# Optimization experiments

Measured on AMD Instinct MI355X. Metric: run time of the kernel, lower is better.

## Reference

```python
import jax, jax.numpy as jnp
import numpy as np

NEG = -1e30  # mask value safe for logsumexp/max
HALF_POS = 4   # positive window: [t-4, t+4)
HALF_ALL = 16  # combined window: [t-16, t+16) (pos + 12 negatives each side)


def _normalize(x, axis=-1, eps=1e-12):
    # matches torch F.normalize: x / max(||x||, eps)
    n = jnp.linalg.norm(x, axis=axis, keepdims=True)
    return x / jnp.maximum(n, eps)


def _banded_logits(q, k, temperature):
    # q, k: [B, T, D] (normalized). Returns logits [B, T, W], valid mask, pos mask.
    B, T, D = q.shape
    offsets = jnp.arange(-HALF_ALL, HALF_ALL)          # [W=32]
    j = jnp.arange(T)[:, None] + offsets[None, :]      # [T, W] absolute indices
    valid = (j >= 0) & (j < T)                         # combined (pos+neg) window
    jc = jnp.clip(j, 0, T - 1)
    kg = k[:, jc, :]                                   # [B, T, W, D]
    logits = jnp.einsum('btd,btwd->btw', q, kg) / temperature
    pos = valid & (offsets >= -HALF_POS)[None, :] & (offsets < HALF_POS)[None, :]
    return logits, valid, pos


def _direction(q, k, temperature):
    logits, valid, pos = _banded_logits(q, k, temperature)
    lse_all = jax.nn.logsumexp(jnp.where(valid, logits, NEG), axis=2)  # [B, T]
    lse_pos = jax.nn.logsumexp(jnp.where(pos, logits, NEG), axis=2)    # [B, T]
    # per-t loss is mean over batch; summed over t
    loss_sum = jnp.sum(jnp.mean(lse_all - lse_pos, axis=0))
    max_all = jnp.max(jnp.where(valid, logits, NEG), axis=2)
    max_pos = jnp.max(jnp.where(pos, logits, NEG), axis=2)
    # argmax falls in positive block (positives listed first -> ties go positive)
    correct = jnp.sum((max_pos >= max_all).astype(jnp.float32))
    return loss_sum, correct


def setup_inputs() -> dict:
    key = jax.random.key(0)
    k1, k2 = jax.random.split(key)
    B, T, D = 16, 4096, 128
    return {
        'motion_feature': jax.random.normal(k1, (B, T, D), dtype=jnp.float32),
        'audio_feature': jax.random.normal(k2, (B, T, D), dtype=jnp.float32),
    }


def reference(motion_feature, audio_feature):
    temperature = 0.1
    B, T, D = motion_feature.shape
    m = _normalize(motion_feature, axis=2)
    a = _normalize(audio_feature, axis=2)
    m2a_loss, m2a_correct = _direction(m, a, temperature)
    a2m_loss, a2m_correct = _direction(a, m, temperature)
    final_loss = (m2a_loss + a2m_loss) / (2 * T)
    total_correct = (m2a_correct + a2m_correct) / (2 * T * B)
    return final_loss, total_correct
```

## Files before the change

### kernel.cpp

```cpp
#include <hip/hip_runtime.h>
#include <hip/hip_bf16.h>

typedef __attribute__((ext_vector_type(8))) short bf16x8;
typedef __attribute__((ext_vector_type(4))) float f32x4;

#define T_DIM 4096
#define B_DIM 16
#define D_DIM 128
#define TILE 64
#define NTILE 4
#define ROWS 96
#define SROW 136
#define NEGV -1e30f
#define NBLK 256
#define SCALE (1.0f / 131072.0f)

#define LDS_BARRIER() asm volatile("s_waitcnt lgkmcnt(0)\n\ts_barrier" ::: "memory")

__global__ __launch_bounds__(512, 2) void lcl_main(
    const float* __restrict__ mot, const float* __restrict__ aud,
    float* __restrict__ ws)
{
    __shared__ unsigned short sm[ROWS * SROW];
    __shared__ unsigned short sa[ROWS * SROW];
    __shared__ float invM[ROWS], invA[ROWS];
    __shared__ float redL[8], redC[8];

    const int tid  = threadIdx.x;
    const int lane = tid & 63;
    const int wv   = tid >> 6;
    const int g32  = tid >> 5;
    const int l32  = tid & 31;

    const int lin = blockIdx.x;
    const int swz = (lin & 7) * (NBLK / 8) + (lin >> 3);
    const int by  = swz >> 4;
    const int tg  = swz & 15;
    const int tbase = tg * (NTILE * TILE);
    const size_t base = (size_t)by * (T_DIM * D_DIM);

    const int dir = wv >> 2;
    const int mi  = wv & 3;
    const unsigned short* q = dir ? sa : sm;
    const unsigned short* k = dir ? sm : sa;
    float* invKarr = dir ? invM : invA;
    const float* invQarr = dir ? invA : invM;

    const int fr    = lane & 15;
    const int fch   = (lane >> 4) * 8;
    const int col16 = lane & 15;
    const int g     = lane >> 4;

    float4 vm[6], va[6];
    {
        const size_t off = base + (size_t)(tbase - 16 + g32) * D_DIM + l32 * 4;
        const float* spm = mot + off;
        const float* spa = aud + off;
        #pragma unroll
        for (int i = 0; i < 6; ++i) {
            const bool ok = (unsigned)(tbase - 16 + g32 + 16 * i) < (unsigned)T_DIM;
            vm[i] = make_float4(0.f, 0.f, 0.f, 0.f);
            va[i] = vm[i];
            if (ok) {
                vm[i] = *reinterpret_cast<const float4*>(spm + (size_t)(16 * i) * D_DIM);
                va[i] = *reinterpret_cast<const float4*>(spa + (size_t)(16 * i) * D_DIM);
            }
        }
    }

    float lossW = 0.f, corrW = 0.f;

    #pragma unroll
    for (int tile = 0; tile < NTILE; ++tile) {
        const int t0 = tbase + tile * TILE;

        {
            unsigned short* dpm = sm + g32 * SROW + l32 * 4;
            unsigned short* dpa = sa + g32 * SROW + l32 * 4;
            #pragma unroll
            for (int i = 0; i < 6; ++i) {
                union { __hip_bfloat16 h[4]; uint2 u; } pm, pa;
                pm.h[0] = __float2bfloat16(vm[i].x);
                pm.h[1] = __float2bfloat16(vm[i].y);
                pm.h[2] = __float2bfloat16(vm[i].z);
                pm.h[3] = __float2bfloat16(vm[i].w);
                pa.h[0] = __float2bfloat16(va[i].x);
                pa.h[1] = __float2bfloat16(va[i].y);
                pa.h[2] = __float2bfloat16(va[i].z);
                pa.h[3] = __float2bfloat16(va[i].w);
                *reinterpret_cast<uint2*>(dpm + 16 * i * SROW) = pm.u;
                *reinterpret_cast<uint2*>(dpa + 16 * i * SROW) = pa.u;
            }
        }

        if (tile + 1 < NTILE) {
            const int tn = t0 + TILE;
            const size_t off = base + (size_t)(tn - 16 + g32) * D_DIM + l32 * 4;
            const float* spm = mot + off;
            const float* spa = aud + off;
            #pragma unroll
            for (int i = 0; i < 6; ++i) {
                const bool ok = (unsigned)(tn - 16 + g32 + 16 * i) < (unsigned)T_DIM;
                vm[i] = make_float4(0.f, 0.f, 0.f, 0.f);
                va[i] = vm[i];
                if (ok) {
                    vm[i] = *reinterpret_cast<const float4*>(spm + (size_t)(16 * i) * D_DIM);
                    va[i] = *reinterpret_cast<const float4*>(spa + (size_t)(16 * i) * D_DIM);
                }
            }
        }
        LDS_BARRIER();

        f32x4 acc0 = {0.f,0.f,0.f,0.f}, acc1 = acc0, acc2 = acc0;
        f32x4 n0 = acc0, n1 = acc0;
        const unsigned short* qrow = q + (16 * (mi + 1) + fr) * SROW + fch;
        const unsigned short* k0   = k + ((mi + 0) * 16 + fr) * SROW + fch;
        const unsigned short* k1   = k + ((mi + 1) * 16 + fr) * SROW + fch;
        const unsigned short* k2   = k + ((mi + 2) * 16 + fr) * SROW + fch;
        #pragma unroll
        for (int ks = 0; ks < 4; ++ks) {
            bf16x8 bq = *reinterpret_cast<const bf16x8*>(qrow + ks * 32);
            bf16x8 a0 = *reinterpret_cast<const bf16x8*>(k0   + ks * 32);
            bf16x8 a1 = *reinterpret_cast<const bf16x8*>(k1   + ks * 32);
            bf16x8 a2 = *reinterpret_cast<const bf16x8*>(k2   + ks * 32);
            acc0 = __builtin_amdgcn_mfma_f32_16x16x32_bf16(a0, bq, acc0, 0, 0, 0);
            acc1 = __builtin_amdgcn_mfma_f32_16x16x32_bf16(a1, bq, acc1, 0, 0, 0);
            acc2 = __builtin_amdgcn_mfma_f32_16x16x32_bf16(a2, bq, acc2, 0, 0, 0);
            n0   = __builtin_amdgcn_mfma_f32_16x16x32_bf16(a0, a0, n0, 0, 0, 0);
            if (mi >= 2)
                n1 = __builtin_amdgcn_mfma_f32_16x16x32_bf16(a2, a2, n1, 0, 0, 0);
        }

        if ((col16 >> 2) == g) {
            const int r = col16 & 3;
            invKarr[16 * mi + col16] = 1.0f / fmaxf(sqrtf(n0[r]), 1e-12f);
            if (mi >= 2)
                invKarr[16 * (mi + 2) + col16] = 1.0f / fmaxf(sqrtf(n1[r]), 1e-12f);
        }
        LDS_BARRIER();

        const float scq10 = 10.0f * invQarr[16 * (mi + 1) + col16];
        const f32x4 sck0 = *reinterpret_cast<const f32x4*>(&invKarr[16 * (mi + 0) + 4 * g]);
        const f32x4 sck1 = *reinterpret_cast<const f32x4*>(&invKarr[16 * (mi + 1) + 4 * g]);
        const f32x4 sck2 = *reinterpret_cast<const f32x4*>(&invKarr[16 * (mi + 2) + 4 * g]);

        const int jbase  = t0 - 16 + 16 * mi + 4 * g;
        const int kkbase = 4 * g - col16;

        float lv[12];
        bool  pmk[12];
        float mx = NEGV, mxp = NEGV;
        #pragma unroll
        for (int bb = 0; bb < 3; ++bb) {
            const f32x4 acc = (bb == 0) ? acc0 : ((bb == 1) ? acc1 : acc2);
            const f32x4 sck = (bb == 0) ? sck0 : ((bb == 1) ? sck1 : sck2);
            #pragma unroll
            for (int r = 0; r < 4; ++r) {
                const int kk = kkbase + 16 * bb + r;
                const int jg = jbase  + 16 * bb + r;
                const bool ok = ((unsigned)kk < 32u) && ((unsigned)jg < (unsigned)T_DIM);
                const float li = ok ? acc[r] * (scq10 * sck[r]) : NEGV;
                const bool  pi = ((unsigned)(kk - 12) < 8u);
                lv[bb * 4 + r]  = li;
                pmk[bb * 4 + r] = pi;
                mx  = fmaxf(mx, li);
                mxp = pi ? fmaxf(mxp, li) : mxp;
            }
        }
        mx  = fmaxf(mx,  __shfl_xor(mx,  16));
        mx  = fmaxf(mx,  __shfl_xor(mx,  32));
        mxp = fmaxf(mxp, __shfl_xor(mxp, 16));
        mxp = fmaxf(mxp, __shfl_xor(mxp, 32));

        float s = 0.f, sp = 0.f;
        #pragma unroll
        for (int i = 0; i < 12; ++i) {
            const float e = __expf(lv[i] - mx);
            s  += e;
            sp += pmk[i] ? e : 0.f;
        }
        s  += __shfl_xor(s,  16);  s  += __shfl_xor(s,  32);
        sp += __shfl_xor(sp, 16);  sp += __shfl_xor(sp, 32);

        if (g == 0) {
            lossW += __logf(s / sp);
            corrW += (mxp >= mx) ? 1.0f : 0.0f;
        }
    }

    #pragma unroll
    for (int m = 32; m; m >>= 1) {
        lossW += __shfl_xor(lossW, m);
        corrW += __shfl_xor(corrW, m);
    }
    if (lane == 0) { redL[wv] = lossW; redC[wv] = corrW; }
    __syncthreads();
    if (tid == 0) {
        float L = 0.f, C = 0.f;
        #pragma unroll
        for (int i = 0; i < 8; ++i) { L += redL[i]; C += redC[i]; }
        ws[2 * swz]     = L;
        ws[2 * swz + 1] = C;
    }
}

__global__ __launch_bounds__(256) void lcl_final(
    const float* __restrict__ ws, float* __restrict__ out)
{
    const int tid = threadIdx.x;
    const float2 v = reinterpret_cast<const float2*>(ws)[tid];
    float L = v.x, C = v.y;
    #pragma unroll
    for (int m = 32; m; m >>= 1) { L += __shfl_xor(L, m); C += __shfl_xor(C, m); }
    __shared__ float rl[4], rc[4];
    if ((tid & 63) == 0) { rl[tid >> 6] = L; rc[tid >> 6] = C; }
    __syncthreads();
    if (tid == 0) {
        out[0] = (rl[0] + rl[1] + rl[2] + rl[3]) * SCALE;
        out[1] = (rc[0] + rc[1] + rc[2] + rc[3]) * SCALE;
    }
}

extern "C" void kernel_launch(void* const* d_in, const int* in_sizes, int n_in,
                              void* d_out, int out_size, void* d_ws, size_t ws_size,
                              hipStream_t stream) {
    const float* mot = (const float*)d_in[0];
    const float* aud = (const float*)d_in[1];
    float* out = (float*)d_out;
    float* ws  = (float*)d_ws;

    lcl_main<<<NBLK, 512, 0, stream>>>(mot, aud, ws);
    lcl_final<<<1, 256, 0, stream>>>(ws, out);
}
```

Baseline: 22.09 us.

## Double-buffer LDS tiles and compute norms in-wave via shuffles, dropping a barrier

LDS staging is double-buffered so each tile writes to alternating buffers, and each wave now computes every norm it needs (q and all three k blocks) with extra MFMAs. The norms are distributed with shuffles instead of being exchanged through shared memory. This removes the second block-wide barrier per tile and the shared inverse-norm arrays. Interior blocks also skip the bounds checks on global loads. The cost is more MFMA work, double the LDS footprint (about 104KB), and rsqrt in place of sqrt plus divide.

```diff
diff --git a/kernel.cpp b/kernel.cpp
--- a/kernel.cpp
+++ b/kernel.cpp
@@ -11,6 +11,7 @@
 #define NTILE 4
 #define ROWS 96
 #define SROW 136
+#define TBUF (ROWS * SROW)
 #define NEGV -1e30f
 #define NBLK 256
 #define SCALE (1.0f / 131072.0f)
@@ -21,9 +22,7 @@
     const float* __restrict__ mot, const float* __restrict__ aud,
     float* __restrict__ ws)
 {
-    __shared__ unsigned short sm[ROWS * SROW];
-    __shared__ unsigned short sa[ROWS * SROW];
-    __shared__ float invM[ROWS], invA[ROWS];
+    __shared__ unsigned short sbuf[2 * 2 * TBUF];
     __shared__ float redL[8], redC[8];
 
     const int tid  = threadIdx.x;
@@ -38,13 +37,10 @@
     const int tg  = swz & 15;
     const int tbase = tg * (NTILE * TILE);
     const size_t base = (size_t)by * (T_DIM * D_DIM);
+    const bool edge = (tg == 0) || (tg == 15);
 
     const int dir = wv >> 2;
     const int mi  = wv & 3;
-    const unsigned short* q = dir ? sa : sm;
-    const unsigned short* k = dir ? sm : sa;
-    float* invKarr = dir ? invM : invA;
-    const float* invQarr = dir ? invA : invM;
 
     const int fr    = lane & 15;
     const int fch   = (lane >> 4) * 8;
@@ -52,31 +48,44 @@
     const int g     = lane >> 4;
 
     float4 vm[6], va[6];
-    {
-        const size_t off = base + (size_t)(tbase - 16 + g32) * D_DIM + l32 * 4;
+    auto issue = [&](int tstart) {
+        const size_t off = base + (size_t)(tstart - 16 + g32) * D_DIM + l32 * 4;
         const float* spm = mot + off;
         const float* spa = aud + off;
-        #pragma unroll
-        for (int i = 0; i < 6; ++i) {
-            const bool ok = (unsigned)(tbase - 16 + g32 + 16 * i) < (unsigned)T_DIM;
-            vm[i] = make_float4(0.f, 0.f, 0.f, 0.f);
-            va[i] = vm[i];
-            if (ok) {
+        if (!edge) {
+            #pragma unroll
+            for (int i = 0; i < 6; ++i) {
                 vm[i] = *reinterpret_cast<const float4*>(spm + (size_t)(16 * i) * D_DIM);
                 va[i] = *reinterpret_cast<const float4*>(spa + (size_t)(16 * i) * D_DIM);
             }
-        }
-    }
+        } else {
+            #pragma unroll
+            for (int i = 0; i < 6; ++i) {
+                const bool ok = (unsigned)(tstart - 16 + g32 + 16 * i) < (unsigned)T_DIM;
+                vm[i] = make_float4(0.f, 0.f, 0.f, 0.f);
+                va[i] = vm[i];
+                if (ok) {
+                    vm[i] = *reinterpret_cast<const float4*>(spm + (size_t)(16 * i) * D_DIM);
+                    va[i] = *reinterpret_cast<const float4*>(spa + (size_t)(16 * i) * D_DIM);
+                }
+            }
+        }
+    };
+
+    issue(tbase);
 
     float lossW = 0.f, corrW = 0.f;
 
     #pragma unroll
     for (int tile = 0; tile < NTILE; ++tile) {
-        const int t0 = tbase + tile * TILE;
+        const int t0  = tbase + tile * TILE;
+        const int cur = tile & 1;
+        unsigned short* smc = sbuf + (cur * 2 + 0) * TBUF;
+        unsigned short* sac = sbuf + (cur * 2 + 1) * TBUF;
 
         {
-            unsigned short* dpm = sm + g32 * SROW + l32 * 4;
-            unsigned short* dpa = sa + g32 * SROW + l32 * 4;
+            unsigned short* dpm = smc + g32 * SROW + l32 * 4;
+            unsigned short* dpa = sac + g32 * SROW + l32 * 4;
             #pragma unroll
             for (int i = 0; i < 6; ++i) {
                 union { __hip_bfloat16 h[4]; uint2 u; } pm, pa;
@@ -93,26 +102,14 @@
             }
         }
 
-        if (tile + 1 < NTILE) {
-            const int tn = t0 + TILE;
-            const size_t off = base + (size_t)(tn - 16 + g32) * D_DIM + l32 * 4;
-            const float* spm = mot + off;
-            const float* spa = aud + off;
-            #pragma unroll
-            for (int i = 0; i < 6; ++i) {
-                const bool ok = (unsigned)(tn - 16 + g32 + 16 * i) < (unsigned)T_DIM;
-                vm[i] = make_float4(0.f, 0.f, 0.f, 0.f);
-                va[i] = vm[i];
-                if (ok) {
-                    vm[i] = *reinterpret_cast<const float4*>(spm + (size_t)(16 * i) * D_DIM);
-                    va[i] = *reinterpret_cast<const float4*>(spa + (size_t)(16 * i) * D_DIM);
-                }
-            }
-        }
+        if (tile + 1 < NTILE) issue(t0 + TILE);
+
         LDS_BARRIER();
 
+        const unsigned short* q = (dir ? sac : smc);
+        const unsigned short* k = (dir ? smc : sac);
         f32x4 acc0 = {0.f,0.f,0.f,0.f}, acc1 = acc0, acc2 = acc0;
-        f32x4 n0 = acc0, n1 = acc0;
+        f32x4 n0 = acc0, n1 = acc0, n2 = acc0, nq = acc0;
         const unsigned short* qrow = q + (16 * (mi + 1) + fr) * SROW + fch;
         const unsigned short* k0   = k + ((mi + 0) * 16 + fr) * SROW + fch;
         const unsigned short* k1   = k + ((mi + 1) * 16 + fr) * SROW + fch;
@@ -127,22 +124,30 @@
             acc1 = __builtin_amdgcn_mfma_f32_16x16x32_bf16(a1, bq, acc1, 0, 0, 0);
             acc2 = __builtin_amdgcn_mfma_f32_16x16x32_bf16(a2, bq, acc2, 0, 0, 0);
             n0   = __builtin_amdgcn_mfma_f32_16x16x32_bf16(a0, a0, n0, 0, 0, 0);
-            if (mi >= 2)
-                n1 = __builtin_amdgcn_mfma_f32_16x16x32_bf16(a2, a2, n1, 0, 0, 0);
-        }
-
-        if ((col16 >> 2) == g) {
-            const int r = col16 & 3;
-            invKarr[16 * mi + col16] = 1.0f / fmaxf(sqrtf(n0[r]), 1e-12f);
-            if (mi >= 2)
-                invKarr[16 * (mi + 2) + col16] = 1.0f / fmaxf(sqrtf(n1[r]), 1e-12f);
-        }
-        LDS_BARRIER();
-
-        const float scq10 = 10.0f * invQarr[16 * (mi + 1) + col16];
-        const f32x4 sck0 = *reinterpret_cast<const f32x4*>(&invKarr[16 * (mi + 0) + 4 * g]);
-        const f32x4 sck1 = *reinterpret_cast<const f32x4*>(&invKarr[16 * (mi + 1) + 4 * g]);
-        const f32x4 sck2 = *reinterpret_cast<const f32x4*>(&invKarr[16 * (mi + 2) + 4 * g]);
+            n1   = __builtin_amdgcn_mfma_f32_16x16x32_bf16(a1, a1, n1, 0, 0, 0);
+            n2   = __builtin_amdgcn_mfma_f32_16x16x32_bf16(a2, a2, n2, 0, 0, 0);
+            nq   = __builtin_amdgcn_mfma_f32_16x16x32_bf16(bq, bq, nq, 0, 0, 0);
+        }
+
+        const int rs = col16 & 3;
+        const float dq = (rs == 0) ? nq[0] : (rs == 1) ? nq[1] : (rs == 2) ? nq[2] : nq[3];
+        const float d0 = (rs == 0) ? n0[0] : (rs == 1) ? n0[1] : (rs == 2) ? n0[2] : n0[3];
+        const float d1 = (rs == 0) ? n1[0] : (rs == 1) ? n1[1] : (rs == 2) ? n1[2] : n1[3];
+        const float d2 = (rs == 0) ? n2[0] : (rs == 1) ? n2[1] : (rs == 2) ? n2[2] : n2[3];
+        const float iq = rsqrtf(fmaxf(dq, 1e-24f));
+        const float i0 = rsqrtf(fmaxf(d0, 1e-24f));
+        const float i1 = rsqrtf(fmaxf(d1, 1e-24f));
+        const float i2 = rsqrtf(fmaxf(d2, 1e-24f));
+
+        const float scq10 = 10.0f * __shfl(iq, col16 + 16 * (col16 >> 2));
+        const int srcn = 20 * g;
+        f32x4 sck0, sck1, sck2;
+        #pragma unroll
+        for (int r = 0; r < 4; ++r) {
+            sck0[r] = __shfl(i0, srcn + r);
+            sck1[r] = __shfl(i1, srcn + r);
+            sck2[r] = __shfl(i2, srcn + r);
+        }
 
         const int jbase  = t0 - 16 + 16 * mi + 4 * g;
         const int kkbase = 4 * g - col16;
```

Measured after the change: 21.44 us. 2.9% less time.
